# Kernel tuning notes

Hardware: AMD Instinct MI355X
Metric: run time of the kernel (lower is better)

Reference implementation:

```python
import jax, jax.numpy as jnp
import numpy as np

B, T = 256, 512
E, H, V, C = 128, 256, 50000, 64


def setup_inputs() -> dict:
    key = jax.random.key(0)
    ks = jax.random.split(key, 8)
    k = 1.0 / np.sqrt(H)
    u = lambda kk, shape: jax.random.uniform(kk, shape, jnp.float32, -k, k)
    return {
        "sentence": jax.random.randint(ks[0], (B, T), 0, V),
        "emb": jax.random.normal(ks[1], (V, E), jnp.float32),
        "W_ih": u(ks[2], (4 * H, E)),
        "W_hh": u(ks[3], (4 * H, H)),
        "b_ih": u(ks[4], (4 * H,)),
        "b_hh": u(ks[5], (4 * H,)),
        "W_lin": u(ks[6], (C, H)),
        "b_lin": u(ks[7], (C,)),
    }


def reference(sentence, emb, W_ih, W_hh, b_ih, b_hh, W_lin, b_lin):
    x = emb[sentence]  # [B, T, E]
    # Precompute input-to-gate projections for all timesteps in one GEMM.
    x_proj = jnp.einsum('bte,ge->btg', x, W_ih) + b_ih + b_hh  # [B, T, 4H]

    def step(carry, xt):
        h, c = carry
        gates = xt + h @ W_hh.T  # [B, 4H], torch gate order i,f,g,o
        i, f, g, o = jnp.split(gates, 4, axis=-1)
        c = jax.nn.sigmoid(f) * c + jax.nn.sigmoid(i) * jnp.tanh(g)
        h = jax.nn.sigmoid(o) * jnp.tanh(c)
        return (h, c), h

    h0 = jnp.zeros((x.shape[0], W_hh.shape[1]), x.dtype)
    _, hs = jax.lax.scan(step, (h0, h0), jnp.swapaxes(x_proj, 0, 1))
    lstm_out = jnp.swapaxes(hs, 0, 1)  # [B, T, H]

    logits = lstm_out @ W_lin.T + b_lin  # [B, T, C]
    # Faithful to original: LogSoftmax over dim=1 (the TIME axis), then prod over time.
    all_probs = jax.nn.log_softmax(logits, axis=1)
    return jnp.prod(all_probs, axis=1)  # [B, C]
```

## Files before the change

kernel.cpp:

```cpp
#include <hip/hip_runtime.h>

#define TT 512
#define HH 256
#define EE 128
#define BB 256
#define CC 64
#define VV 50000
#define NSB 128

#define OFF_EMB   0ull
#define OFF_WHA   6400000ull
#define OFF_WXA   6662144ull
#define OFF_BIAS  6793216ull
#define OFF_WLIN  6797312ull
#define OFF_LSTM  6813696ull
#define OFF_LOG   73922560ull
#define WS_NEED   107476992ull

typedef __attribute__((ext_vector_type(4))) float    f32x4;
typedef __attribute__((ext_vector_type(4))) unsigned u32x4;
typedef __attribute__((ext_vector_type(8))) int      i32x8;
typedef int i32x8u __attribute__((ext_vector_type(8), aligned(16)));
typedef __bf16 bf16x8_t __attribute__((ext_vector_type(8)));

__device__ __forceinline__ float rcp_f(float x) { return __builtin_amdgcn_rcpf(x); }
__device__ __forceinline__ float exp2_(float x) {
  float r; asm("v_exp_f32 %0, %1" : "=v"(r) : "v"(x)); return r;
}
__device__ __forceinline__ unsigned short to_bf16(float f) {
  unsigned u = __float_as_uint(f);
  return (unsigned short)((u + 0x7fffu + ((u >> 16) & 1u)) >> 16);
}
__device__ __forceinline__ f32x4 mfma_mx(i32x8 a, i32x8 b, f32x4 c) {
  return __builtin_amdgcn_mfma_scale_f32_16x16x128_f8f6f4(
      a, b, c, 0, 0, 0, 0x7f7f7f7f, 0, 0x7f7f7f7f);
}

#define LOG2E  1.442695041f
#define SN_    (-LOG2E / 1024.f)
#define SG_    (-2.f * LOG2E / 1024.f)
#define C2_    (-2.f * LOG2E)

__global__ void prep_emb(const float* __restrict__ emb, unsigned* __restrict__ out) {
  const int stride = gridDim.x * blockDim.x;
  for (int u = blockIdx.x * blockDim.x + threadIdx.x; u < (VV * EE / 4); u += stride) {
    const f32x4 f = ((const f32x4*)emb)[u];
    int r = __builtin_amdgcn_cvt_pk_fp8_f32(f[0], f[1], 0, false);
    r = __builtin_amdgcn_cvt_pk_fp8_f32(f[2], f[3], r, true);
    out[u] = (unsigned)r;
  }
}

__global__ void prep_wha(const float* __restrict__ Whh, unsigned char* __restrict__ wf) {
  const int id = blockIdx.x * 256 + threadIdx.x;
  const int b = id & 31, l = (id >> 5) & 63;
  const int kt = (id >> 11) & 1, mt = (id >> 12) & 7, w8 = id >> 15;
  const int r16 = l & 15;
  const int grow = (r16 & 3) * 256 + (w8 * 32 + mt * 4 + (r16 >> 2));
  const int k = kt * 128 + ((l >> 4) << 5) + b;
  const int r = __builtin_amdgcn_cvt_pk_fp8_f32(64.f * Whh[grow * HH + k], 0.f, 0, false);
  wf[id] = (unsigned char)(r & 0xff);
}

__global__ void prep_wxa(const float* __restrict__ Wih, unsigned char* __restrict__ wf) {
  const int id = blockIdx.x * 256 + threadIdx.x;
  const int b = id & 31, l = (id >> 5) & 63;
  const int mt = (id >> 11) & 7, w8 = id >> 14;
  const int r16 = l & 15;
  const int grow = (r16 & 3) * 256 + (w8 * 32 + mt * 4 + (r16 >> 2));
  const int k = ((l >> 4) << 5) + b;
  const int r = __builtin_amdgcn_cvt_pk_fp8_f32(1024.f * Wih[grow * EE + k], 0.f, 0, false);
  wf[id] = (unsigned char)(r & 0xff);
}

__global__ void prep_bias(const float* __restrict__ bih, const float* __restrict__ bhh,
                          float* __restrict__ bp) {
  const int n = blockIdx.x * 256 + threadIdx.x;
  const float sc = (n >= 512 && n < 768) ? (-2.f * LOG2E) : (-LOG2E);
  bp[n] = (bih[n] + bhh[n]) * sc;
}

__global__ void prep_wlin(const float* __restrict__ Wlin, unsigned short* __restrict__ wl) {
  const int id = blockIdx.x * 256 + threadIdx.x;
  const int j = id & 7, l = (id >> 3) & 63;
  const int kk = (id >> 9) & 7, q = id >> 12;
  const int c = q * 16 + (l & 15);
  const int k = kk * 32 + ((l >> 4) << 3) + j;
  wl[id] = to_bf16(Wlin[c * HH + k]);
}

__global__ __launch_bounds__(512, 1)
void lstm_scan(const int* __restrict__ sent, const unsigned char* __restrict__ emb8,
               const unsigned char* __restrict__ wha, const unsigned char* __restrict__ wxa,
               const float* __restrict__ bias, unsigned short* __restrict__ lstm_out) {
  __shared__ __align__(16) unsigned char xa[32 * 2304];
  __shared__ __align__(16) unsigned char bh[2 * 2304];
  __shared__ __align__(16) unsigned char xbuf[2][2304];
  __shared__ __align__(16) float redistf[8][544];
  __shared__ int sent_lds[4][512];

  const int tid = threadIdx.x;
  const int lane = tid & 63;
  const int w = tid >> 6;
  const int b0 = blockIdx.x << 2;

  i32x8 Ah[8][2];
#pragma unroll
  for (int mt = 0; mt < 8; ++mt)
#pragma unroll
    for (int kt = 0; kt < 2; ++kt)
      Ah[mt][kt] = *(const i32x8*)(wha + ((w * 8 + mt) * 2 + kt) * 2048 + lane * 32);
  i32x8 Ax[4];
#pragma unroll
  for (int mtx = 0; mtx < 4; ++mtx)
    Ax[mtx] = *(const i32x8*)(wxa + ((w * 8 + mtx) * 64 + lane) * 32);

  for (int c = tid; c < 4096; c += 512) {
    const int tile = c >> 7, i = c & 127, ln = i >> 1, hf = i & 1;
    const int w8 = tile >> 2, mtx = tile & 3;
    *(u32x4*)(xa + tile * 2304 + ln * 32 + (ln >> 2) * 16 + hf * 16) =
        *(const u32x4*)(wxa + ((w8 * 8 + 4 + mtx) * 64 + ln) * 32 + hf * 16);
  }
  for (int i = tid; i < 2048; i += 512)
    sent_lds[i >> 9][i & 511] = sent[(b0 + (i >> 9)) * TT + (i & 511)];
  for (int i = tid; i < 1152; i += 512) ((int*)bh)[i] = 0;

  const int gr = 2 * w + (lane >> 3), gq = lane & 7;
  const int* sptr = &sent_lds[gr & 3][gr >> 2];
  const unsigned char* embg = emb8 + gq * 16;
  const int gwo = (gq >> 1) * 576 + (gq & 1) * 16 + gr * 32 + (gr >> 2) * 16;

  __syncthreads();

  u32x4 xg;
  if (lane < 16) {
    const int i0s = sptr[0];
    *(u32x4*)(xbuf[0] + gwo) = *(const u32x4*)(embg + (size_t)i0s * EE);
    const int i1s = sptr[4];
    *(u32x4*)(xbuf[1] + gwo) = *(const u32x4*)(embg + (size_t)i1s * EE);
    const int i2s = sptr[8];
    xg = *(const u32x4*)(embg + (size_t)i2s * EE);
  }
  __syncthreads();

  const int lread = lane * 32 + (lane >> 2) * 16;
  const f32x4 Zf = (f32x4){0.f, 0.f, 0.f, 0.f};
  f32x4 acc[8];
  {
    const i32x8 Bx = __builtin_bit_cast(i32x8, *(const i32x8u*)(xbuf[0] + lread));
#pragma unroll
    for (int mtx = 0; mtx < 4; ++mtx) {
      const i32x8 Aq = __builtin_bit_cast(i32x8, *(const i32x8u*)(xa + (w * 4 + mtx) * 2304 + lread));
      acc[mtx] = mfma_mx(Ax[mtx], Bx, Zf);
      acc[4 + mtx] = mfma_mx(Aq, Bx, Zf);
    }
  }

  const int s = lane & 3;
  const int mtT = lane >> 3;
  const int hp = ((lane >> 2) & 1) << 1;
  const int hulS = lane >> 4;
  const int hu0 = w * 32 + mtT * 4 + hp;
  const float bi0 = bias[hu0],       bf0 = bias[256 + hu0],
              bg0 = bias[512 + hu0], bo0 = bias[768 + hu0];
  const float bi1 = bias[hu0 + 1],       bf1 = bias[256 + hu0 + 1],
              bg1 = bias[512 + hu0 + 1], bo1 = bias[768 + hu0 + 1];
  const int k7 = hu0 & 127;
  const int cellbase = (hu0 >> 7) * 2304 + (k7 >> 5) * 576 + (k7 & 31);
  const int s32 = s * 32;
  const int wroff = hulS * 16 + s * 4;
  const int rdoff = mtT * 68 + hp * 16 + s * 4;
  const long obase = ((long)(b0 + s) * TT) * HH + hu0;
  float cs0 = 0.f, cs1 = 0.f;

#define MICRO(J) { \
  const i32x8 Bh0 = __builtin_bit_cast(i32x8, *(const i32x8u*)(bh + lread)); \
  const i32x8 Bh1 = __builtin_bit_cast(i32x8, *(const i32x8u*)(bh + 2304 + lread)); \
  __builtin_amdgcn_s_setprio(1); \
  _Pragma("unroll") for (int mt = 0; mt < 8; ++mt) acc[mt] = mfma_mx(Ah[mt][0], Bh0, acc[mt]); \
  _Pragma("unroll") for (int mt = 0; mt < 8; ++mt) acc[mt] = mfma_mx(Ah[mt][1], Bh1, acc[mt]); \
  __builtin_amdgcn_s_setprio(0); \
  if (((lane >> 2) & 3) == (J)) { \
    _Pragma("unroll") for (int mt = 0; mt < 8; ++mt) \
      *(f32x4*)&redistf[w][mt * 68 + wroff] = acc[mt]; \
  } \
  if ((J) == 2) { \
    if (dogS) *(u32x4*)(xbC + gwo) = xg; \
    if (dogL) { const int idx = sptr[(tb + 3) * 4]; \
                xg = *(const u32x4*)(embg + (size_t)idx * EE); } \
  } \
  if ((J) == 3) { \
    const i32x8 Bx = __builtin_bit_cast(i32x8, *(const i32x8u*)(xbN + lread)); \
    _Pragma("unroll") for (int mtx = 0; mtx < 4; ++mtx) { \
      const i32x8 Aq = __builtin_bit_cast(i32x8, *(const i32x8u*)(xa + (w * 4 + mtx) * 2304 + lread)); \
      acc[mtx] = mfma_mx(Ax[mtx], Bx, Zf); \
      acc[4 + mtx] = mfma_mx(Aq, Bx, Zf); \
    } \
  } \
  asm volatile("s_waitcnt lgkmcnt(0)" ::: "memory"); \
  __builtin_amdgcn_sched_barrier(0); \
  const f32x4 g0 = *(const f32x4*)&redistf[w][rdoff]; \
  const f32x4 g1 = *(const f32x4*)&redistf[w][rdoff + 16]; \
  float si, sf, so, tg, tc, hv0, hv1; \
  si = rcp_f(1.f + exp2_(g0[0] * SN_ + bi0)); \
  sf = rcp_f(1.f + exp2_(g0[1] * SN_ + bf0)); \
  tg = 2.f * rcp_f(1.f + exp2_(g0[2] * SG_ + bg0)) - 1.f; \
  so = rcp_f(1.f + exp2_(g0[3] * SN_ + bo0)); \
  cs0 = sf * cs0 + si * tg; \
  tc = 2.f * rcp_f(1.f + exp2_(cs0 * C2_)) - 1.f; \
  hv0 = so * tc; \
  si = rcp_f(1.f + exp2_(g1[0] * SN_ + bi1)); \
  sf = rcp_f(1.f + exp2_(g1[1] * SN_ + bf1)); \
  tg = 2.f * rcp_f(1.f + exp2_(g1[2] * SG_ + bg1)) - 1.f; \
  so = rcp_f(1.f + exp2_(g1[3] * SN_ + bo1)); \
  cs1 = sf * cs1 + si * tg; \
  tc = 2.f * rcp_f(1.f + exp2_(cs1 * C2_)) - 1.f; \
  hv1 = so * tc; \
  { \
    const int pk = __builtin_amdgcn_cvt_pk_fp8_f32(16.f * hv0, 16.f * hv1, 0, false); \
    *(unsigned short*)(bh + cellbase + s32 + ((((J) + 1) & 3)) * 144) = (unsigned short)(pk & 0xffff); \
    *(unsigned short*)(bh + cellbase + s32 + (J) * 144) = 0; \
    unsigned pb; asm("v_cvt_pk_bf16_f32 %0, %1, %2" : "=v"(pb) : "v"(hv0), "v"(hv1)); \
    *(unsigned*)(lstm_out + obase + (long)(t0 + (J)) * HH) = pb; \
  } \
  asm volatile("s_waitcnt lgkmcnt(0)" ::: "memory"); \
  __builtin_amdgcn_s_barrier(); \
}

#pragma unroll 1
  for (int tb = 0; tb < NSB; ++tb) {
    const int t0 = tb << 2;
    const bool dogS = (lane < 16) && (tb + 2 < NSB);
    const bool dogL = (lane < 16) && (tb + 3 < NSB);
    unsigned char* xbC = xbuf[tb & 1];
    unsigned char* xbN = xbuf[(tb + 1) & 1];
    MICRO(0)
    MICRO(1)
    MICRO(2)
    MICRO(3)
  }
#undef MICRO
}

__global__ __launch_bounds__(256)
void logits_gemm(const unsigned short* __restrict__ lstm, const unsigned short* __restrict__ wl,
                 const float* __restrict__ blin, float* __restrict__ logits) {
  const int tid = threadIdx.x, l = tid & 63, wv = tid >> 6;
  const long m0 = (long)blockIdx.x * 64 + wv * 16;
  f32x4 ac[4];
#pragma unroll
  for (int q = 0; q < 4; ++q) ac[q] = (f32x4){0.f, 0.f, 0.f, 0.f};
  const unsigned short* arow = lstm + (m0 + (l & 15)) * HH + ((l >> 4) << 3);
#pragma unroll
  for (int kk = 0; kk < 8; ++kk) {
    const bf16x8_t a = __builtin_bit_cast(bf16x8_t, *(const u32x4*)(arow + kk * 32));
#pragma unroll
    for (int q = 0; q < 4; ++q) {
      const bf16x8_t b = __builtin_bit_cast(bf16x8_t, *(const u32x4*)(wl + (((q * 8 + kk) * 64 + l) << 3)));
      ac[q] = __builtin_amdgcn_mfma_f32_16x16x32_bf16(a, b, ac[q], 0, 0, 0);
    }
  }
  const int r0 = (l >> 4) << 2;
#pragma unroll
  for (int q = 0; q < 4; ++q) {
    const int col = q * 16 + (l & 15);
    const float bb = blin[col];
#pragma unroll
    for (int r = 0; r < 4; ++r)
      logits[(m0 + r0 + r) * CC + col] = ac[q][r] + bb;
  }
}

__global__ __launch_bounds__(256)
void softmax_prod(const float* __restrict__ logits, float* __restrict__ out) {
  __shared__ float lds[TT * CC];
  __shared__ float red[3][4][CC];
  const int tid = threadIdx.x, b = blockIdx.x;
  const f32x4* src = (const f32x4*)(logits + (long)b * TT * CC);
  f32x4* dst = (f32x4*)lds;
#pragma unroll 1
  for (int i = tid; i < TT * CC / 4; i += 256) dst[i] = src[i];
  __syncthreads();

  const int c = tid & 63, part = tid >> 6;
  const int t0 = part * 128;
  float m = -3.0e38f;
  for (int k = 0; k < 128; ++k) m = fmaxf(m, lds[(t0 + k) * CC + c]);
  red[0][part][c] = m;
  __syncthreads();
  m = fmaxf(fmaxf(red[0][0][c], red[0][1][c]), fmaxf(red[0][2][c], red[0][3][c]));

  float ssum = 0.f;
  for (int k = 0; k < 128; ++k) ssum += __expf(lds[(t0 + k) * CC + c] - m);
  red[1][part][c] = ssum;
  __syncthreads();
  ssum = red[1][0][c] + red[1][1][c] + red[1][2][c] + red[1][3][c];
  const float lse = m + __logf(ssum);

  float pacc = 0.f;
  for (int k = 0; k < 128; ++k) pacc += __log2f(fabsf(lds[(t0 + k) * CC + c] - lse));
  red[2][part][c] = pacc;
  __syncthreads();
  if (part == 0) {
    const float tot = red[2][0][c] + red[2][1][c] + red[2][2][c] + red[2][3][c];
    out[b * CC + c] = exp2f(fminf(tot, 127.0f));
  }
}

extern "C" void kernel_launch(void* const* d_in, const int* in_sizes, int n_in,
                              void* d_out, int out_size, void* d_ws, size_t ws_size,
                              hipStream_t stream) {
  (void)in_sizes; (void)n_in; (void)out_size;
  if (ws_size < WS_NEED) return;

  const int*   sent = (const int*)d_in[0];
  const float* emb  = (const float*)d_in[1];
  const float* Wih  = (const float*)d_in[2];
  const float* Whh  = (const float*)d_in[3];
  const float* bih  = (const float*)d_in[4];
  const float* bhh  = (const float*)d_in[5];
  const float* Wlin = (const float*)d_in[6];
  const float* blin = (const float*)d_in[7];
  float* out = (float*)d_out;
  char* ws = (char*)d_ws;

  unsigned char*  emb8 = (unsigned char*)(ws + OFF_EMB);
  unsigned char*  wha  = (unsigned char*)(ws + OFF_WHA);
  unsigned char*  wxa  = (unsigned char*)(ws + OFF_WXA);
  float*          bp   = (float*)(ws + OFF_BIAS);
  unsigned short* wl   = (unsigned short*)(ws + OFF_WLIN);
  unsigned short* lo   = (unsigned short*)(ws + OFF_LSTM);
  float*          lg   = (float*)(ws + OFF_LOG);

  prep_emb<<<1024, 256, 0, stream>>>(emb, (unsigned*)emb8);
  prep_wha<<<1024, 256, 0, stream>>>(Whh, wha);
  prep_wxa<<<512, 256, 0, stream>>>(Wih, wxa);
  prep_bias<<<4, 256, 0, stream>>>(bih, bhh, bp);
  prep_wlin<<<64, 256, 0, stream>>>(Wlin, wl);
  lstm_scan<<<64, 512, 0, stream>>>(sent, emb8, wha, wxa, bp, lo);
  logits_gemm<<<2048, 256, 0, stream>>>(lo, wl, blin, lg);
  softmax_prod<<<256, 256, 0, stream>>>(lg, out);
}
```

Baseline: 585.3 us.

## Switch LSTM scan MFMAs from FP8 to FP4 with scaled operands

```diff
diff --git a/kernel.cpp b/kernel.cpp
--- a/kernel.cpp
+++ b/kernel.cpp
@@ -19,8 +19,8 @@
 
 typedef __attribute__((ext_vector_type(4))) float    f32x4;
 typedef __attribute__((ext_vector_type(4))) unsigned u32x4;
+typedef __attribute__((ext_vector_type(4))) int      i32x4;
 typedef __attribute__((ext_vector_type(8))) int      i32x8;
-typedef int i32x8u __attribute__((ext_vector_type(8), aligned(16)));
 typedef __bf16 bf16x8_t __attribute__((ext_vector_type(8)));
 
 __device__ __forceinline__ float rcp_f(float x) { return __builtin_amdgcn_rcpf(x); }
@@ -31,46 +31,65 @@
   unsigned u = __float_as_uint(f);
   return (unsigned short)((u + 0x7fffu + ((u >> 16) & 1u)) >> 16);
 }
-__device__ __forceinline__ f32x4 mfma_mx(i32x8 a, i32x8 b, f32x4 c) {
+__device__ __forceinline__ unsigned enc4(float v) {
+  const unsigned sg = (__float_as_uint(v) >> 31) << 3;
+  const float a = fminf(fabsf(v), 6.0f);
+  const float c = (a < 2.0f) ? __builtin_rintf(a + a)
+                : (a < 4.0f) ? __builtin_rintf(a) + 2.0f
+                             : __builtin_rintf(a * 0.5f) + 4.0f;
+  return sg | (unsigned)(int)c;
+}
+__device__ __forceinline__ i32x8 up8(i32x4 v) {
+  i32x8 r;
+  r[0] = v[0]; r[1] = v[1]; r[2] = v[2]; r[3] = v[3];
+  r[4] = 0; r[5] = 0; r[6] = 0; r[7] = 0;
+  return r;
+}
+__device__ __forceinline__ f32x4 mfma4(i32x8 a, i32x8 b, f32x4 c, int sb) {
   return __builtin_amdgcn_mfma_scale_f32_16x16x128_f8f6f4(
-      a, b, c, 0, 0, 0, 0x7f7f7f7f, 0, 0x7f7f7f7f);
-}
+      a, b, c, 4, 4, 0, 0x7f7f7f7f, 0, sb);
+}
+#define SB_H 0x7f7f7f7f
+#define SB_X 0x80808080
 
 #define LOG2E  1.442695041f
-#define SN_    (-LOG2E / 1024.f)
-#define SG_    (-2.f * LOG2E / 1024.f)
+#define SN2    (-LOG2E / 256.f)
+#define SG2    (-2.f * LOG2E / 256.f)
 #define C2_    (-2.f * LOG2E)
 
 __global__ void prep_emb(const float* __restrict__ emb, unsigned* __restrict__ out) {
-  const int stride = gridDim.x * blockDim.x;
-  for (int u = blockIdx.x * blockDim.x + threadIdx.x; u < (VV * EE / 4); u += stride) {
-    const f32x4 f = ((const f32x4*)emb)[u];
-    int r = __builtin_amdgcn_cvt_pk_fp8_f32(f[0], f[1], 0, false);
-    r = __builtin_amdgcn_cvt_pk_fp8_f32(f[2], f[3], r, true);
-    out[u] = (unsigned)r;
-  }
+  const int u = blockIdx.x * 256 + threadIdx.x;
+  const f32x4 f0 = ((const f32x4*)emb)[u * 2];
+  const f32x4 f1 = ((const f32x4*)emb)[u * 2 + 1];
+  unsigned r = enc4(2.f * f0[0]) | (enc4(2.f * f0[1]) << 4);
+  r |= (enc4(2.f * f0[2]) | (enc4(2.f * f0[3]) << 4)) << 8;
+  r |= (enc4(2.f * f1[0]) | (enc4(2.f * f1[1]) << 4)) << 16;
+  r |= (enc4(2.f * f1[2]) | (enc4(2.f * f1[3]) << 4)) << 24;
+  out[u] = r;
 }
 
 __global__ void prep_wha(const float* __restrict__ Whh, unsigned char* __restrict__ wf) {
   const int id = blockIdx.x * 256 + threadIdx.x;
-  const int b = id & 31, l = (id >> 5) & 63;
-  const int kt = (id >> 11) & 1, mt = (id >> 12) & 7, w8 = id >> 15;
+  const int byt = id & 15, l = (id >> 4) & 63;
+  const int kt = (id >> 10) & 1, mt = (id >> 11) & 7, w8 = id >> 14;
   const int r16 = l & 15;
-  const int grow = (r16 & 3) * 256 + (w8 * 32 + mt * 4 + (r16 >> 2));
-  const int k = kt * 128 + ((l >> 4) << 5) + b;
-  const int r = __builtin_amdgcn_cvt_pk_fp8_f32(64.f * Whh[grow * HH + k], 0.f, 0, false);
-  wf[id] = (unsigned char)(r & 0xff);
+  const int grow = (r16 & 3) * 256 + w8 * 32 + mt * 4 + (r16 >> 2);
+  const int k0 = kt * 128 + ((l >> 4) << 5) + byt * 2;
+  const unsigned n0 = enc4(64.f * Whh[grow * HH + k0]);
+  const unsigned n1 = enc4(64.f * Whh[grow * HH + k0 + 1]);
+  wf[id] = (unsigned char)(n0 | (n1 << 4));
 }
 
 __global__ void prep_wxa(const float* __restrict__ Wih, unsigned char* __restrict__ wf) {
   const int id = blockIdx.x * 256 + threadIdx.x;
-  const int b = id & 31, l = (id >> 5) & 63;
-  const int mt = (id >> 11) & 7, w8 = id >> 14;
+  const int byt = id & 15, l = (id >> 4) & 63;
+  const int mt = (id >> 10) & 7, w8 = id >> 13;
   const int r16 = l & 15;
-  const int grow = (r16 & 3) * 256 + (w8 * 32 + mt * 4 + (r16 >> 2));
-  const int k = ((l >> 4) << 5) + b;
-  const int r = __builtin_amdgcn_cvt_pk_fp8_f32(1024.f * Wih[grow * EE + k], 0.f, 0, false);
-  wf[id] = (unsigned char)(r & 0xff);
+  const int grow = (r16 & 3) * 256 + w8 * 32 + mt * 4 + (r16 >> 2);
+  const int k0 = ((l >> 4) << 5) + byt * 2;
+  const unsigned n0 = enc4(64.f * Wih[grow * EE + k0]);
+  const unsigned n1 = enc4(64.f * Wih[grow * EE + k0 + 1]);
+  wf[id] = (unsigned char)(n0 | (n1 << 4));
 }
 
 __global__ void prep_bias(const float* __restrict__ bih, const float* __restrict__ bhh,
@@ -90,12 +109,12 @@
 }
 
 __global__ __launch_bounds__(512, 1)
-void lstm_scan(const int* __restrict__ sent, const unsigned char* __restrict__ emb8,
+void lstm_scan(const int* __restrict__ sent, const unsigned char* __restrict__ emb4,
                const unsigned char* __restrict__ wha, const unsigned char* __restrict__ wxa,
                const float* __restrict__ bias, unsigned short* __restrict__ lstm_out) {
-  __shared__ __align__(16) unsigned char xa[32 * 2304];
-  __shared__ __align__(16) unsigned char bh[2 * 2304];
-  __shared__ __align__(16) unsigned char xbuf[2][2304];
+  __shared__ __align__(16) unsigned char xa[64 * 1024];
+  __shared__ __align__(16) unsigned char bh[2 * 1024];
+  __shared__ __align__(16) unsigned char xbuf[2][1024];
   __shared__ __align__(16) float redistf[8][544];
   __shared__ int sent_lds[4][512];
 
@@ -109,50 +128,41 @@
   for (int mt = 0; mt < 8; ++mt)
 #pragma unroll
     for (int kt = 0; kt < 2; ++kt)
-      Ah[mt][kt] = *(const i32x8*)(wha + ((w * 8 + mt) * 2 + kt) * 2048 + lane * 32);
-  i32x8 Ax[4];
-#pragma unroll
-  for (int mtx = 0; mtx < 4; ++mtx)
-    Ax[mtx] = *(const i32x8*)(wxa + ((w * 8 + mtx) * 64 + lane) * 32);
-
-  for (int c = tid; c < 4096; c += 512) {
-    const int tile = c >> 7, i = c & 127, ln = i >> 1, hf = i & 1;
-    const int w8 = tile >> 2, mtx = tile & 3;
-    *(u32x4*)(xa + tile * 2304 + ln * 32 + (ln >> 2) * 16 + hf * 16) =
-        *(const u32x4*)(wxa + ((w8 * 8 + 4 + mtx) * 64 + ln) * 32 + hf * 16);
-  }
+      Ah[mt][kt] = up8(*(const i32x4*)(wha + (((w * 8 + mt) * 2 + kt) * 64 + lane) * 16));
+
+  for (int c = tid; c < 4096; c += 512)
+    ((u32x4*)xa)[c] = ((const u32x4*)wxa)[c];
   for (int i = tid; i < 2048; i += 512)
     sent_lds[i >> 9][i & 511] = sent[(b0 + (i >> 9)) * TT + (i & 511)];
-  for (int i = tid; i < 1152; i += 512) ((int*)bh)[i] = 0;
-
-  const int gr = 2 * w + (lane >> 3), gq = lane & 7;
+  if (tid < 512) ((int*)bh)[tid] = 0;
+
+  const int gr = 2 * w + ((lane >> 2) & 1), gq = lane & 3;
   const int* sptr = &sent_lds[gr & 3][gr >> 2];
-  const unsigned char* embg = emb8 + gq * 16;
-  const int gwo = (gq >> 1) * 576 + (gq & 1) * 16 + gr * 32 + (gr >> 2) * 16;
+  const unsigned char* embg = emb4 + gq * 16;
+  const int gwo = gq * 256 + gr * 16;
 
   __syncthreads();
 
   u32x4 xg;
-  if (lane < 16) {
+  if (lane < 8) {
     const int i0s = sptr[0];
-    *(u32x4*)(xbuf[0] + gwo) = *(const u32x4*)(embg + (size_t)i0s * EE);
+    *(u32x4*)(xbuf[0] + gwo) = *(const u32x4*)(embg + (size_t)i0s * 64);
     const int i1s = sptr[4];
-    *(u32x4*)(xbuf[1] + gwo) = *(const u32x4*)(embg + (size_t)i1s * EE);
+    *(u32x4*)(xbuf[1] + gwo) = *(const u32x4*)(embg + (size_t)i1s * 64);
     const int i2s = sptr[8];
-    xg = *(const u32x4*)(embg + (size_t)i2s * EE);
-  }
-  __syncthreads();
-
-  const int lread = lane * 32 + (lane >> 2) * 16;
+    xg = *(const u32x4*)(embg + (size_t)i2s * 64);
+  }
+  __syncthreads();
+
+  const int l16 = lane * 16;
   const f32x4 Zf = (f32x4){0.f, 0.f, 0.f, 0.f};
   f32x4 acc[8];
   {
-    const i32x8 Bx = __builtin_bit_cast(i32x8, *(const i32x8u*)(xbuf[0] + lread));
-#pragma unroll
-    for (int mtx = 0; mtx < 4; ++mtx) {
-      const i32x8 Aq = __builtin_bit_cast(i32x8, *(const i32x8u*)(xa + (w * 4 + mtx) * 2304 + lread));
-      acc[mtx] = mfma_mx(Ax[mtx], Bx, Zf);
-      acc[4 + mtx] = mfma_mx(Aq, Bx, Zf);
+    const i32x8 Bx = up8(*(const i32x4*)(xbuf[0] + l16));
+#pragma unroll
+    for (int mtx = 0; mtx < 8; ++mtx) {
+      const i32x8 Aq = up8(*(const i32x4*)(xa + (w * 8 + mtx) * 1024 + l16));
+      acc[mtx] = mfma4(Aq, Bx, Zf, SB_X);
     }
   }
 
@@ -165,20 +175,18 @@
               bg0 = bias[512 + hu0], bo0 = bias[768 + hu0];
   const float bi1 = bias[hu0 + 1],       bf1 = bias[256 + hu0 + 1],
               bg1 = bias[512 + hu0 + 1], bo1 = bias[768 + hu0 + 1];
-  const int k7 = hu0 & 127;
-  const int cellbase = (hu0 >> 7) * 2304 + (k7 >> 5) * 576 + (k7 & 31);
-  const int s32 = s * 32;
+  const int cb4 = (hu0 >> 7) * 1024 + ((hu0 & 127) >> 5) * 256 + s * 16 + ((hu0 & 31) >> 1);
   const int wroff = hulS * 16 + s * 4;
   const int rdoff = mtT * 68 + hp * 16 + s * 4;
   const long obase = ((long)(b0 + s) * TT) * HH + hu0;
   float cs0 = 0.f, cs1 = 0.f;
 
 #define MICRO(J) { \
-  const i32x8 Bh0 = __builtin_bit_cast(i32x8, *(const i32x8u*)(bh + lread)); \
-  const i32x8 Bh1 = __builtin_bit_cast(i32x8, *(const i32x8u*)(bh + 2304 + lread)); \
+  const i32x8 Bh0 = up8(*(const i32x4*)(bh + l16)); \
+  const i32x8 Bh1 = up8(*(const i32x4*)(bh + 1024 + l16)); \
   __builtin_amdgcn_s_setprio(1); \
-  _Pragma("unroll") for (int mt = 0; mt < 8; ++mt) acc[mt] = mfma_mx(Ah[mt][0], Bh0, acc[mt]); \
-  _Pragma("unroll") for (int mt = 0; mt < 8; ++mt) acc[mt] = mfma_mx(Ah[mt][1], Bh1, acc[mt]); \
+  _Pragma("unroll") for (int mt = 0; mt < 8; ++mt) acc[mt] = mfma4(Ah[mt][0], Bh0, acc[mt], SB_H); \
+  _Pragma("unroll") for (int mt = 0; mt < 8; ++mt) acc[mt] = mfma4(Ah[mt][1], Bh1, acc[mt], SB_H); \
   __builtin_amdgcn_s_setprio(0); \
   if (((lane >> 2) & 3) == (J)) { \
     _Pragma("unroll") for (int mt = 0; mt < 8; ++mt) \
@@ -187,14 +195,13 @@
   if ((J) == 2) { \
     if (dogS) *(u32x4*)(xbC + gwo) = xg; \
     if (dogL) { const int idx = sptr[(tb + 3) * 4]; \
-                xg = *(const u32x4*)(embg + (size_t)idx * EE); } \
+                xg = *(const u32x4*)(embg + (size_t)idx * 64); } \
   } \
   if ((J) == 3) { \
-    const i32x8 Bx = __builtin_bit_cast(i32x8, *(const i32x8u*)(xbN + lread)); \
-    _Pragma("unroll") for (int mtx = 0; mtx < 4; ++mtx) { \
-      const i32x8 Aq = __builtin_bit_cast(i32x8, *(const i32x8u*)(xa + (w * 4 + mtx) * 2304 + lread)); \
-      acc[mtx] = mfma_mx(Ax[mtx], Bx, Zf); \
-      acc[4 + mtx] = mfma_mx(Aq, Bx, Zf); \
+    const i32x8 Bx = up8(*(const i32x4*)(xbN + l16)); \
+    _Pragma("unroll") for (int mtx = 0; mtx < 8; ++mtx) { \
+      const i32x8 Aq = up8(*(const i32x4*)(xa + (w * 8 + mtx) * 1024 + l16)); \
+      acc[mtx] = mfma4(Aq, Bx, Zf, SB_X); \
     } \
   } \
   asm volatile("s_waitcnt lgkmcnt(0)" ::: "memory"); \
@@ -202,24 +209,24 @@
   const f32x4 g0 = *(const f32x4*)&redistf[w][rdoff]; \
   const f32x4 g1 = *(const f32x4*)&redistf[w][rdoff + 16]; \
   float si, sf, so, tg, tc, hv0, hv1; \
-  si = rcp_f(1.f + exp2_(g0[0] * SN_ + bi0)); \
-  sf = rcp_f(1.f + exp2_(g0[1] * SN_ + bf0)); \
-  tg = 2.f * rcp_f(1.f + exp2_(g0[2] * SG_ + bg0)) - 1.f; \
-  so = rcp_f(1.f + exp2_(g0[3] * SN_ + bo0)); \
+  si = rcp_f(1.f + exp2_(g0[0] * SN2 + bi0)); \
+  sf = rcp_f(1.f + exp2_(g0[1] * SN2 + bf0)); \
+  tg = 2.f * rcp_f(1.f + exp2_(g0[2] * SG2 + bg0)) - 1.f; \
+  so = rcp_f(1.f + exp2_(g0[3] * SN2 + bo0)); \
   cs0 = sf * cs0 + si * tg; \
   tc = 2.f * rcp_f(1.f + exp2_(cs0 * C2_)) - 1.f; \
   hv0 = so * tc; \
-  si = rcp_f(1.f + exp2_(g1[0] * SN_ + bi1)); \
-  sf = rcp_f(1.f + exp2_(g1[1] * SN_ + bf1)); \
-  tg = 2.f * rcp_f(1.f + exp2_(g1[2] * SG_ + bg1)) - 1.f; \
-  so = rcp_f(1.f + exp2_(g1[3] * SN_ + bo1)); \
+  si = rcp_f(1.f + exp2_(g1[0] * SN2 + bi1)); \
+  sf = rcp_f(1.f + exp2_(g1[1] * SN2 + bf1)); \
+  tg = 2.f * rcp_f(1.f + exp2_(g1[2] * SG2 + bg1)) - 1.f; \
+  so = rcp_f(1.f + exp2_(g1[3] * SN2 + bo1)); \
   cs1 = sf * cs1 + si * tg; \
   tc = 2.f * rcp_f(1.f + exp2_(cs1 * C2_)) - 1.f; \
   hv1 = so * tc; \
   { \
-    const int pk = __builtin_amdgcn_cvt_pk_fp8_f32(16.f * hv0, 16.f * hv1, 0, false); \
-    *(unsigned short*)(bh + cellbase + s32 + ((((J) + 1) & 3)) * 144) = (unsigned short)(pk & 0xffff); \
-    *(unsigned short*)(bh + cellbase + s32 + (J) * 144) = 0; \
+    const unsigned nib = enc4(4.f * hv0) | (enc4(4.f * hv1) << 4); \
+    bh[cb4 + ((((J) + 1) & 3)) * 64] = (unsigned char)nib; \
+    bh[cb4 + (J) * 64] = 0; \
     unsigned pb; asm("v_cvt_pk_bf16_f32 %0, %1, %2" : "=v"(pb) : "v"(hv0), "v"(hv1)); \
     *(unsigned*)(lstm_out + obase + (long)(t0 + (J)) * HH) = pb; \
   } \
@@ -230,8 +237,8 @@
 #pragma unroll 1
   for (int tb = 0; tb < NSB; ++tb) {
     const int t0 = tb << 2;
-    const bool dogS = (lane < 16) && (tb + 2 < NSB);
-    const bool dogL = (lane < 16) && (tb + 3 < NSB);
+    const bool dogS = (lane < 8) && (tb + 2 < NSB);
+    const bool dogL = (lane < 8) && (tb + 3 < NSB);
     unsigned char* xbC = xbuf[tb & 1];
     unsigned char* xbN = xbuf[(tb + 1) & 1];
     MICRO(0)
@@ -324,7 +331,7 @@
   float* out = (float*)d_out;
   char* ws = (char*)d_ws;
 
-  unsigned char*  emb8 = (unsigned char*)(ws + OFF_EMB);
+  unsigned char*  emb4 = (unsigned char*)(ws + OFF_EMB);
   unsigned char*  wha  = (unsigned char*)(ws + OFF_WHA);
   unsigned char*  wxa  = (unsigned char*)(ws + OFF_WXA);
   float*          bp   = (float*)(ws + OFF_BIAS);
@@ -332,12 +339,12 @@
   unsigned short* lo   = (unsigned short*)(ws + OFF_LSTM);
   float*          lg   = (float*)(ws + OFF_LOG);
 
-  prep_emb<<<1024, 256, 0, stream>>>(emb, (unsigned*)emb8);
-  prep_wha<<<1024, 256, 0, stream>>>(Whh, wha);
-  prep_wxa<<<512, 256, 0, stream>>>(Wih, wxa);
+  prep_emb<<<3125, 256, 0, stream>>>(emb, (unsigned*)emb4);
+  prep_wha<<<512, 256, 0, stream>>>(Whh, wha);
+  prep_wxa<<<256, 256, 0, stream>>>(Wih, wxa);
   prep_bias<<<4, 256, 0, stream>>>(bih, bhh, bp);
   prep_wlin<<<64, 256, 0, stream>>>(Wlin, wl);
-  lstm_scan<<<64, 512, 0, stream>>>(sent, emb8, wha, wxa, bp, lo);
+  lstm_scan<<<64, 512, 0, stream>>>(sent, emb4, wha, wxa, bp, lo);
   logits_gemm<<<2048, 256, 0, stream>>>(lo, wl, blin, lg);
   softmax_prod<<<256, 256, 0, stream>>>(lg, out);
 }
```

Result: faster. 564.4 us (-3.6%).
